# Optimization experiments

Measured on AMD Instinct MI355X. Metric: run time of the kernel, lower is better.

## Reference

```python
import jax, jax.numpy as jnp
import numpy as np

SPATIAL_SHAPES = np.array([[128, 128], [64, 64], [32, 32], [16, 16]], dtype=np.int32)  # (H, W) per level
D_MODEL = 256
D_FFN = 1024
N_LEVELS = 4
N_HEADS = 8
N_POINTS = 4
HEAD_DIM = D_MODEL // N_HEADS
B = 2
LEN = int((SPATIAL_SHAPES[:, 0] * SPATIAL_SHAPES[:, 1]).sum())  # 21760


def layer_norm(x, g, b, eps=1e-5):
    mu = x.mean(-1, keepdims=True)
    var = ((x - mu) ** 2).mean(-1, keepdims=True)
    return (x - mu) / jnp.sqrt(var + eps) * g + b


def ms_deform_attn_core(value, sampling_locations, attention_weights):
    # value: [B, Len, M, D]; locations: [B, Lq, M, L, P, 2] in [0,1]; weights: [B, Lq, M, L, P]
    B_, _, M, D = value.shape
    Lq = sampling_locations.shape[1]
    P = sampling_locations.shape[4]
    out = jnp.zeros((B_, M, Lq, D), value.dtype)
    start = 0
    for lvl, (H, W) in enumerate(SPATIAL_SHAPES.tolist()):
        v = value[:, start:start + H * W].transpose(0, 2, 1, 3)  # [B, M, H*W, D]
        start += H * W
        loc = sampling_locations[:, :, :, lvl].transpose(0, 2, 1, 3, 4)  # [B, M, Lq, P, 2]
        # grid_sample semantics: align_corners=False, padding_mode='zeros'
        x = loc[..., 0] * W - 0.5
        y = loc[..., 1] * H - 0.5
        x0 = jnp.floor(x)
        y0 = jnp.floor(y)
        wx = (x - x0)[..., None]
        wy = (y - y0)[..., None]

        def gather(xi, yi):
            valid = ((xi >= 0) & (xi < W) & (yi >= 0) & (yi < H)).astype(value.dtype)
            idx = (jnp.clip(yi, 0, H - 1) * W + jnp.clip(xi, 0, W - 1)).astype(jnp.int32)
            idx = idx.reshape(B_, M, Lq * P)
            g = jnp.take_along_axis(v, idx[..., None], axis=2).reshape(B_, M, Lq, P, D)
            return g * valid[..., None]

        v00 = gather(x0, y0)
        v01 = gather(x0 + 1, y0)
        v10 = gather(x0, y0 + 1)
        v11 = gather(x0 + 1, y0 + 1)
        samp = (v00 * (1 - wx) + v01 * wx) * (1 - wy) + (v10 * (1 - wx) + v11 * wx) * wy
        w_l = attention_weights[:, :, :, lvl].transpose(0, 2, 1, 3)  # [B, M, Lq, P]
        out = out + (samp * w_l[..., None]).sum(axis=3)
    return out.transpose(0, 2, 1, 3).reshape(B_, Lq, M * D)


def setup_inputs() -> dict:
    key = jax.random.key(0)
    ks = jax.random.split(key, 16)
    f32 = jnp.float32

    def lin(k, fan_in, fan_out, scale=None):
        s = scale if scale is not None else 1.0 / np.sqrt(fan_in)
        return jax.random.normal(k, (fan_in, fan_out), f32) * s

    starts = np.concatenate([[0], np.cumsum(SPATIAL_SHAPES[:, 0] * SPATIAL_SHAPES[:, 1])[:-1]]).astype(np.int32)
    inp = {
        "src": jax.random.normal(ks[0], (B, LEN, D_MODEL), f32),
        "pos": jax.random.normal(ks[1], (B, LEN, D_MODEL), f32),
        "reference_points": jax.random.uniform(ks[2], (B, LEN, N_LEVELS, 2), f32),
        "spatial_shapes": jnp.asarray(SPATIAL_SHAPES),
        "level_start_index": jnp.asarray(starts),
        "norm1_g": jnp.ones((D_MODEL,), f32), "norm1_b": jnp.zeros((D_MODEL,), f32),
        "norm2_g": jnp.ones((D_MODEL,), f32), "norm2_b": jnp.zeros((D_MODEL,), f32),
        "W_value": lin(ks[3], D_MODEL, D_MODEL), "b_value": jnp.zeros((D_MODEL,), f32),
        "W_off": lin(ks[4], D_MODEL, N_HEADS * N_LEVELS * N_POINTS * 2, scale=0.01),
        "b_off": jax.random.normal(ks[5], (N_HEADS * N_LEVELS * N_POINTS * 2,), f32) * 0.01,
        "W_attn": lin(ks[6], D_MODEL, N_HEADS * N_LEVELS * N_POINTS),
        "b_attn": jnp.zeros((N_HEADS * N_LEVELS * N_POINTS,), f32),
        "W_out": lin(ks[7], D_MODEL, D_MODEL), "b_out": jnp.zeros((D_MODEL,), f32),
        "W_ffn1": lin(ks[8], D_MODEL, D_FFN), "b_ffn1": jnp.zeros((D_FFN,), f32),
        "W_ffn2": lin(ks[9], D_FFN, D_MODEL), "b_ffn2": jnp.zeros((D_MODEL,), f32),
    }
    return inp


def reference(src, pos, reference_points, spatial_shapes, level_start_index,
              norm1_g, norm1_b, norm2_g, norm2_b,
              W_value, b_value, W_off, b_off, W_attn, b_attn, W_out, b_out,
              W_ffn1, b_ffn1, W_ffn2, b_ffn2):
    B_, Lq, C = src.shape
    # pre-norm deformable self-attention; NOTE: value path uses un-normed src (faithful to source)
    q = layer_norm(src, norm1_g, norm1_b) + pos
    value = (src @ W_value + b_value).reshape(B_, Lq, N_HEADS, HEAD_DIM)
    offsets = (q @ W_off + b_off).reshape(B_, Lq, N_HEADS, N_LEVELS, N_POINTS, 2)
    attn = jax.nn.softmax((q @ W_attn + b_attn).reshape(B_, Lq, N_HEADS, N_LEVELS * N_POINTS), axis=-1)
    attn = attn.reshape(B_, Lq, N_HEADS, N_LEVELS, N_POINTS)
    offset_normalizer = spatial_shapes[..., ::-1].astype(src.dtype)  # (W, H) per level
    loc = reference_points[:, :, None, :, None, :] + offsets / offset_normalizer[None, None, None, :, None, :]
    attn_out = ms_deform_attn_core(value, loc, attn) @ W_out + b_out
    src = src + attn_out
    h = layer_norm(src, norm2_g, norm2_b)
    h = jax.nn.gelu(h @ W_ffn1 + b_ffn1, approximate=False) @ W_ffn2 + b_ffn2
    return src + h
```

## Files before the change

### kernel.cpp

```cpp
#include <hip/hip_runtime.h>
#include <hip/hip_bf16.h>
#include <math.h>

#define LEN_TOT 21760
#define BATCH 2
#define MROWS (BATCH * LEN_TOT)
#define DMODEL 256
#define DFFN 1024

typedef unsigned short ushort_t;
typedef __attribute__((ext_vector_type(8))) short short8;
typedef __attribute__((ext_vector_type(4))) float floatx4;
typedef __attribute__((address_space(3))) ushort_t lds_us;
typedef __attribute__((address_space(1))) const ushort_t glb_us;

__device__ __forceinline__ ushort_t f2b(float f) {
    unsigned u = __float_as_uint(f);
    unsigned r = (u + 0x7FFFu + ((u >> 16) & 1u)) >> 16;
    return (ushort_t)r;
}

struct TP {
    const float* s[6];
    ushort_t*    d[6];
    int K[6];
    int N[6];
    int start[7];
};

__global__ __launch_bounds__(256) void transpose_convert(TP tp) {
    __shared__ float tile[32][33];
    int blk = blockIdx.x;
    int seg = 0;
    while (seg < 5 && blk >= tp.start[seg + 1]) seg++;
    int local = blk - tp.start[seg];
    int K = tp.K[seg], N = tp.N[seg];
    int tn = N >> 5;
    int k0 = (local / tn) << 5, n0 = (local % tn) << 5;
    int r = threadIdx.x >> 5, c = threadIdx.x & 31;
    const float* src = tp.s[seg];
    #pragma unroll
    for (int rr = r; rr < 32; rr += 8)
        tile[rr][c] = src[(size_t)(k0 + rr) * N + n0 + c];
    __syncthreads();
    ushort_t* dst = tp.d[seg];
    #pragma unroll
    for (int rr = r; rr < 32; rr += 8)
        dst[(size_t)(n0 + rr) * K + k0 + c] = f2b(tile[c][rr]);
}

__global__ __launch_bounds__(256) void ln_dual_kernel(
    const float* __restrict__ x, const float* __restrict__ g,
    const float* __restrict__ bb, const float* __restrict__ addv,
    ushort_t* __restrict__ y_bf, ushort_t* __restrict__ x_bf)
{
    int row  = blockIdx.x * 4 + (threadIdx.x >> 6);
    int lane = threadIdx.x & 63;
    size_t base = (size_t)row * DMODEL + lane * 4;
    float4 v = *(const float4*)(x + base);

    float s = v.x + v.y + v.z + v.w;
    #pragma unroll
    for (int o = 32; o; o >>= 1) s += __shfl_xor(s, o, 64);
    float mu = s * (1.0f / 256.0f);

    float d0 = v.x - mu, d1 = v.y - mu, d2 = v.z - mu, d3 = v.w - mu;
    float vs = d0*d0 + d1*d1 + d2*d2 + d3*d3;
    #pragma unroll
    for (int o = 32; o; o >>= 1) vs += __shfl_xor(vs, o, 64);
    float rstd = rsqrtf(vs * (1.0f / 256.0f) + 1e-5f);

    float4 gv = *(const float4*)(g  + lane * 4);
    float4 bv = *(const float4*)(bb + lane * 4);
    float o0 = d0 * rstd * gv.x + bv.x;
    float o1 = d1 * rstd * gv.y + bv.y;
    float o2 = d2 * rstd * gv.z + bv.z;
    float o3 = d3 * rstd * gv.w + bv.w;
    if (addv) {
        float4 av = *(const float4*)(addv + base);
        o0 += av.x; o1 += av.y; o2 += av.z; o3 += av.w;
    }
    ushort4 ob = {f2b(o0), f2b(o1), f2b(o2), f2b(o3)};
    *(ushort4*)(y_bf + base) = ob;
    if (x_bf) {
        ushort4 xb = {f2b(v.x), f2b(v.y), f2b(v.z), f2b(v.w)};
        *(ushort4*)(x_bf + base) = xb;
    }
}

template<int GELU_ACT, int HAS_RES, int OUT_BF16>
__global__ __launch_bounds__(256) void gemm_mfma(
    const ushort_t* __restrict__ A, const ushort_t* __restrict__ Bt,
    const float* __restrict__ bias, const float* __restrict__ res,
    float* __restrict__ C, ushort_t* __restrict__ Cbf,
    int M, int N, int K)
{
    constexpr int BM = 128, BK = 32;
    __shared__ __align__(16) ushort_t As[BM * BK];
    __shared__ __align__(16) ushort_t Bs[BM * BK];

    const int tid  = threadIdx.x;
    const int wave = tid >> 6;
    const int lane = tid & 63;
    const int wm = (wave & 1) * 64;
    const int wn = (wave >> 1) * 64;
    const int ml = lane & 15;
    const int quad = lane >> 4;
    const int m0 = blockIdx.y * BM, n0 = blockIdx.x * BM;

    const int r0 = tid >> 2, s0 = tid & 3;
    const int r1 = (tid + 256) >> 2;

    floatx4 acc[4][4] = {};

    for (int k0 = 0; k0 < K; k0 += BK) {
        const ushort_t* gA0 = A  + (size_t)(m0 + r0) * K + k0 + s0 * 8;
        const ushort_t* gA1 = A  + (size_t)(m0 + r1) * K + k0 + s0 * 8;
        const ushort_t* gB0 = Bt + (size_t)(n0 + r0) * K + k0 + s0 * 8;
        const ushort_t* gB1 = Bt + (size_t)(n0 + r1) * K + k0 + s0 * 8;
        __builtin_amdgcn_global_load_lds((glb_us*)gA0, (lds_us*)(As + tid * 8),        16, 0, 0);
        __builtin_amdgcn_global_load_lds((glb_us*)gA1, (lds_us*)(As + (tid + 256) * 8),16, 0, 0);
        __builtin_amdgcn_global_load_lds((glb_us*)gB0, (lds_us*)(Bs + tid * 8),        16, 0, 0);
        __builtin_amdgcn_global_load_lds((glb_us*)gB1, (lds_us*)(Bs + (tid + 256) * 8),16, 0, 0);
        __syncthreads();

        short8 af[4], bfr[4];
        #pragma unroll
        for (int i = 0; i < 4; i++)
            af[i] = *(const short8*)(As + (wm + i * 16 + ml) * BK + quad * 8);
        #pragma unroll
        for (int j = 0; j < 4; j++)
            bfr[j] = *(const short8*)(Bs + (wn + j * 16 + ml) * BK + quad * 8);
        #pragma unroll
        for (int i = 0; i < 4; i++)
            #pragma unroll
            for (int j = 0; j < 4; j++)
                acc[i][j] = __builtin_amdgcn_mfma_f32_16x16x32_bf16(
                    af[i], bfr[j], acc[i][j], 0, 0, 0);
        __syncthreads();
    }

    if (OUT_BF16) {
        ushort_t* pool  = (wave < 2) ? As : Bs;
        ushort_t* wbase = pool + (wave & 1) * 2048;
        const int lr  = lane >> 2;
        const int sg  = lane & 3;
        #pragma unroll
        for (int i = 0; i < 4; i++) {
            ushort_t* wbuf = wbase + (i & 1) * 1024;
            #pragma unroll
            for (int j = 0; j < 4; j++) {
                float bc = bias[n0 + wn + j * 16 + ml];
                #pragma unroll
                for (int r = 0; r < 4; r++) {
                    float v = acc[i][j][r] + bc;
                    if (GELU_ACT) v = 0.5f * v * (1.0f + erff(v * 0.7071067811865476f));
                    if (HAS_RES)
                        v += res[(size_t)(m0 + wm + i * 16 + quad * 4 + r) * N
                                 + n0 + wn + j * 16 + ml];
                    wbuf[(quad * 4 + r) * 64 + j * 16 + ml] = f2b(v);
                }
            }
            asm volatile("s_waitcnt lgkmcnt(0)" ::: "memory");
            #pragma unroll
            for (int h = 0; h < 2; h++) {
                short8 vv = *(const short8*)(wbuf + lr * 64 + (sg + 4 * h) * 8);
                *(short8*)(Cbf + (size_t)(m0 + wm + i * 16 + lr) * N
                                 + n0 + wn + (sg + 4 * h) * 8) = vv;
            }
        }
    } else {
        #pragma unroll
        for (int j = 0; j < 4; j++) {
            int col = n0 + wn + j * 16 + ml;
            float bc = bias[col];
            #pragma unroll
            for (int i = 0; i < 4; i++) {
                int row = m0 + wm + i * 16 + quad * 4;
                #pragma unroll
                for (int r = 0; r < 4; r++) {
                    float v = acc[i][j][r] + bc;
                    if (GELU_ACT) v = 0.5f * v * (1.0f + erff(v * 0.7071067811865476f));
                    if (HAS_RES) v += res[(size_t)(row + r) * N + col];
                    C[(size_t)(row + r) * N + col] = v;
                }
            }
        }
    }
}

__global__ __launch_bounds__(256) void msdeform_kernel(
    const float* __restrict__ value, const float* __restrict__ offs,
    const float* __restrict__ logits, const float* __restrict__ refp,
    ushort_t* __restrict__ out_bf)
{
    int gid = blockIdx.x * 8 + (threadIdx.x >> 5);
    int l   = threadIdx.x & 31;
    int bq  = gid >> 3;
    int m   = gid & 7;
    int b   = (bq >= LEN_TOT) ? 1 : 0;

    int i = l & 15;
    float logit = logits[(size_t)gid * 16 + i];
    float mx = logit;
    #pragma unroll
    for (int o = 8; o; o >>= 1) mx = fmaxf(mx, __shfl_xor(mx, o, 32));
    float e = __expf(logit - mx);
    float se = e;
    #pragma unroll
    for (int o = 8; o; o >>= 1) se += __shfl_xor(se, o, 32);
    float prob = e / se;

    int lvl = i >> 2;
    int Wl  = 128 >> lvl;
    float Wf = (float)Wl;
    const int ST_[4] = {0, 16384, 20480, 21504};

    float2 off2 = ((const float2*)offs)[(size_t)gid * 16 + i];
    float2 ref2 = ((const float2*)refp)[(size_t)bq * 4 + lvl];
    float xs = fmaf(ref2.x, Wf, off2.x) - 0.5f;
    float ys = fmaf(ref2.y, Wf, off2.y) - 0.5f;
    float xf = floorf(xs), yf = floorf(ys);
    int x0 = (int)xf, y0 = (int)yf;
    float wx = xs - xf, wy = ys - yf;
    float wx1 = 1.0f - wx, wy1 = 1.0f - wy;

    bool vx0 = (x0 >= 0) & (x0 < Wl);
    bool vx1 = (x0 + 1 >= 0) & (x0 + 1 < Wl);
    bool vy0 = (y0 >= 0) & (y0 < Wl);
    bool vy1 = (y0 + 1 >= 0) & (y0 + 1 < Wl);
    int cx0 = min(max(x0, 0), Wl - 1);
    int cx1 = min(max(x0 + 1, 0), Wl - 1);
    int cy0 = min(max(y0, 0), Wl - 1);
    int cy1 = min(max(y0 + 1, 0), Wl - 1);

    int vbase = b * LEN_TOT + ST_[lvl];
    int i00 = (vbase + cy0 * Wl + cx0) * 256 + m * 32;
    int i01 = (vbase + cy0 * Wl + cx1) * 256 + m * 32;
    int i10 = (vbase + cy1 * Wl + cx0) * 256 + m * 32;
    int i11 = (vbase + cy1 * Wl + cx1) * 256 + m * 32;
    float w00 = (vx0 && vy0) ? prob * wx1 * wy1 : 0.0f;
    float w01 = (vx1 && vy0) ? prob * wx  * wy1 : 0.0f;
    float w10 = (vx0 && vy1) ? prob * wx1 * wy  : 0.0f;
    float w11 = (vx1 && vy1) ? prob * wx  * wy  : 0.0f;

    int sA = l >> 2;
    int cA = l & 3;
    int t0 = __shfl(i00, sA, 32), t1 = __shfl(i01, sA, 32);
    int t2 = __shfl(i10, sA, 32), t3 = __shfl(i11, sA, 32);
    int addrA = (cA == 0) ? t0 : (cA == 1) ? t1 : (cA == 2) ? t2 : t3;
    float u0 = __shfl(w00, sA, 32), u1 = __shfl(w01, sA, 32);
    float u2 = __shfl(w10, sA, 32), u3 = __shfl(w11, sA, 32);
    float wA = (cA == 0) ? u0 : (cA == 1) ? u1 : (cA == 2) ? u2 : u3;
    t0 = __shfl(i00, sA + 8, 32); t1 = __shfl(i01, sA + 8, 32);
    t2 = __shfl(i10, sA + 8, 32); t3 = __shfl(i11, sA + 8, 32);
    int addrB = (cA == 0) ? t0 : (cA == 1) ? t1 : (cA == 2) ? t2 : t3;
    u0 = __shfl(w00, sA + 8, 32); u1 = __shfl(w01, sA + 8, 32);
    u2 = __shfl(w10, sA + 8, 32); u3 = __shfl(w11, sA + 8, 32);
    float wB = (cA == 0) ? u0 : (cA == 1) ? u1 : (cA == 2) ? u2 : u3;

    int cl = l >> 3;
    int d4 = l & 7;
    float ax = 0.0f, ay = 0.0f, az = 0.0f, aw = 0.0f;
    #pragma unroll
    for (int s = 0; s < 8; s++) {
        int   a = __shfl(addrA, s * 4 + cl, 32);
        float w = __shfl(wA,    s * 4 + cl, 32);
        float4 v = *(const float4*)(value + a + (d4 << 2));
        ax = fmaf(w, v.x, ax); ay = fmaf(w, v.y, ay);
        az = fmaf(w, v.z, az); aw = fmaf(w, v.w, aw);
    }
    #pragma unroll
    for (int s = 0; s < 8; s++) {
        int   a = __shfl(addrB, s * 4 + cl, 32);
        float w = __shfl(wB,    s * 4 + cl, 32);
        float4 v = *(const float4*)(value + a + (d4 << 2));
        ax = fmaf(w, v.x, ax); ay = fmaf(w, v.y, ay);
        az = fmaf(w, v.z, az); aw = fmaf(w, v.w, aw);
    }
    ax += __shfl_xor(ax, 8, 32);  ay += __shfl_xor(ay, 8, 32);
    az += __shfl_xor(az, 8, 32);  aw += __shfl_xor(aw, 8, 32);
    ax += __shfl_xor(ax, 16, 32); ay += __shfl_xor(ay, 16, 32);
    az += __shfl_xor(az, 16, 32); aw += __shfl_xor(aw, 16, 32);

    if (l < 8) {
        ushort4 o = {f2b(ax), f2b(ay), f2b(az), f2b(aw)};
        *(ushort4*)(out_bf + (size_t)gid * 32 + (d4 << 2)) = o;
    }
}

extern "C" void kernel_launch(void* const* d_in, const int* in_sizes, int n_in,
                              void* d_out, int out_size, void* d_ws, size_t ws_size,
                              hipStream_t stream)
{
    const float* src  = (const float*)d_in[0];
    const float* pos  = (const float*)d_in[1];
    const float* refp = (const float*)d_in[2];
    const float* n1g = (const float*)d_in[5];
    const float* n1b = (const float*)d_in[6];
    const float* n2g = (const float*)d_in[7];
    const float* n2b = (const float*)d_in[8];
    const float* Wv  = (const float*)d_in[9];
    const float* bv  = (const float*)d_in[10];
    const float* Wof = (const float*)d_in[11];
    const float* bof = (const float*)d_in[12];
    const float* Wat = (const float*)d_in[13];
    const float* bat = (const float*)d_in[14];
    const float* Wo  = (const float*)d_in[15];
    const float* bo  = (const float*)d_in[16];
    const float* Wf1 = (const float*)d_in[17];
    const float* bf1 = (const float*)d_in[18];
    const float* Wf2 = (const float*)d_in[19];
    const float* bf2 = (const float*)d_in[20];
    float* out = (float*)d_out;

    char* ws = (char*)d_ws;
    const int M = MROWS;
    const size_t SZ_BF = (size_t)M * 256 * 2;
    const size_t SZ_F  = (size_t)M * 256 * 4;

    ushort_t* q_bf    = (ushort_t*)(ws);
    float*    value   = (float*)   (ws + SZ_BF);
    ushort_t* src_bf  = (ushort_t*)(ws + SZ_BF + SZ_F);
    float*    offsb   = (float*)   (ws + 2 * SZ_BF + SZ_F);
    float*    logitsb = (float*)   (ws + 2 * SZ_BF + 2 * SZ_F);
    ushort_t* h0_bf   = q_bf;
    ushort_t* sampled = src_bf;
    float*    src2    = value;
    ushort_t* h1_bf   = src_bf;
    char* wtp = ws + 2 * SZ_BF + 2 * SZ_F + (size_t)M * 128 * 4;
    ushort_t* WvT  = (ushort_t*)(wtp);
    ushort_t* WofT = WvT  + 256 * 256;
    ushort_t* WatT = WofT + 256 * 256;
    ushort_t* WoT  = WatT + 256 * 128;
    ushort_t* Wf1T = WoT  + 256 * 256;
    ushort_t* Wf2T = Wf1T + 256 * 1024;

    TP tp;
    tp.s[0] = Wv;  tp.d[0] = WvT;  tp.K[0] = 256;  tp.N[0] = 256;
    tp.s[1] = Wof; tp.d[1] = WofT; tp.K[1] = 256;  tp.N[1] = 256;
    tp.s[2] = Wat; tp.d[2] = WatT; tp.K[2] = 256;  tp.N[2] = 128;
    tp.s[3] = Wo;  tp.d[3] = WoT;  tp.K[3] = 256;  tp.N[3] = 256;
    tp.s[4] = Wf1; tp.d[4] = Wf1T; tp.K[4] = 256;  tp.N[4] = 1024;
    tp.s[5] = Wf2; tp.d[5] = Wf2T; tp.K[5] = 1024; tp.N[5] = 256;
    tp.start[0] = 0;   tp.start[1] = 64;  tp.start[2] = 128;
    tp.start[3] = 160; tp.start[4] = 224; tp.start[5] = 480; tp.start[6] = 736;
    transpose_convert<<<736, 256, 0, stream>>>(tp);

    ln_dual_kernel<<<M / 4, 256, 0, stream>>>(src, n1g, n1b, pos, q_bf, src_bf);
    gemm_mfma<0, 0, 0><<<dim3(2, M / 128), 256, 0, stream>>>(
        src_bf, WvT, bv, nullptr, value, nullptr, M, 256, 256);
    gemm_mfma<0, 0, 0><<<dim3(2, M / 128), 256, 0, stream>>>(
        q_bf, WofT, bof, nullptr, offsb, nullptr, M, 256, 256);
    gemm_mfma<0, 0, 0><<<dim3(1, M / 128), 256, 0, stream>>>(
        q_bf, WatT, bat, nullptr, logitsb, nullptr, M, 128, 256);
    msdeform_kernel<<<M, 256, 0, stream>>>(value, offsb, logitsb, refp, sampled);
    gemm_mfma<0, 1, 0><<<dim3(2, M / 128), 256, 0, stream>>>(
        sampled, WoT, bo, src, src2, nullptr, M, 256, 256);
    ln_dual_kernel<<<M / 4, 256, 0, stream>>>(src2, n2g, n2b, nullptr, h0_bf, nullptr);
    gemm_mfma<1, 0, 1><<<dim3(8, M / 128), 256, 0, stream>>>(
        h0_bf, Wf1T, bf1, nullptr, nullptr, h1_bf, M, 1024, 256);
    gemm_mfma<0, 1, 0><<<dim3(2, M / 128), 256, 0, stream>>>(
        h1_bf, Wf2T, bf2, src2, out, nullptr, M, 256, 1024);
}
```

Measured before the change: 506.8 us.

## Fuse offset and attention-logit GEMMs and store value projection in bf16

The offset and attention-logit projections become one GEMM with N=384, which relies on WofT and WatT being contiguous and uses a split bias. Its output is a combined row-major buffer that the deformable-attention kernel indexes directly. The value projection now writes bf16 instead of fp32, which halves the gather traffic in msdeform_kernel, and loads are widened back to float in registers. The cost is lower precision in the sampled values and an extra branch on bias selection in every GEMM epilogue.

```diff
diff --git a/kernel.cpp b/kernel.cpp
--- a/kernel.cpp
+++ b/kernel.cpp
@@ -18,6 +18,9 @@
     unsigned u = __float_as_uint(f);
     unsigned r = (u + 0x7FFFu + ((u >> 16) & 1u)) >> 16;
     return (ushort_t)r;
+}
+__device__ __forceinline__ float b2f(ushort_t u) {
+    return __uint_as_float(((unsigned)u) << 16);
 }
 
 struct TP {
@@ -91,7 +94,8 @@
 template<int GELU_ACT, int HAS_RES, int OUT_BF16>
 __global__ __launch_bounds__(256) void gemm_mfma(
     const ushort_t* __restrict__ A, const ushort_t* __restrict__ Bt,
-    const float* __restrict__ bias, const float* __restrict__ res,
+    const float* __restrict__ bias, const float* __restrict__ bias2, int bsplit,
+    const float* __restrict__ res,
     float* __restrict__ C, ushort_t* __restrict__ Cbf,
     int M, int N, int K)
 {
@@ -150,7 +154,8 @@
             ushort_t* wbuf = wbase + (i & 1) * 1024;
             #pragma unroll
             for (int j = 0; j < 4; j++) {
-                float bc = bias[n0 + wn + j * 16 + ml];
+                int col = n0 + wn + j * 16 + ml;
+                float bc = (col < bsplit) ? bias[col] : bias2[col - bsplit];
                 #pragma unroll
                 for (int r = 0; r < 4; r++) {
                     float v = acc[i][j][r] + bc;
@@ -173,7 +178,7 @@
         #pragma unroll
         for (int j = 0; j < 4; j++) {
             int col = n0 + wn + j * 16 + ml;
-            float bc = bias[col];
+            float bc = (col < bsplit) ? bias[col] : bias2[col - bsplit];
             #pragma unroll
             for (int i = 0; i < 4; i++) {
                 int row = m0 + wm + i * 16 + quad * 4;
@@ -190,9 +195,8 @@
 }
 
 __global__ __launch_bounds__(256) void msdeform_kernel(
-    const float* __restrict__ value, const float* __restrict__ offs,
-    const float* __restrict__ logits, const float* __restrict__ refp,
-    ushort_t* __restrict__ out_bf)
+    const ushort_t* __restrict__ value, const float* __restrict__ comb,
+    const float* __restrict__ refp, ushort_t* __restrict__ out_bf)
 {
     int gid = blockIdx.x * 8 + (threadIdx.x >> 5);
     int l   = threadIdx.x & 31;
@@ -201,7 +205,7 @@
     int b   = (bq >= LEN_TOT) ? 1 : 0;
 
     int i = l & 15;
-    float logit = logits[(size_t)gid * 16 + i];
+    float logit = comb[(size_t)bq * 384 + 256 + m * 16 + i];
     float mx = logit;
     #pragma unroll
     for (int o = 8; o; o >>= 1) mx = fmaxf(mx, __shfl_xor(mx, o, 32));
@@ -216,7 +220,7 @@
     float Wf = (float)Wl;
     const int ST_[4] = {0, 16384, 20480, 21504};
 
-    float2 off2 = ((const float2*)offs)[(size_t)gid * 16 + i];
+    float2 off2 = ((const float2*)comb)[(size_t)bq * 192 + m * 16 + i];
     float2 ref2 = ((const float2*)refp)[(size_t)bq * 4 + lvl];
     float xs = fmaf(ref2.x, Wf, off2.x) - 0.5f;
     float ys = fmaf(ref2.y, Wf, off2.y) - 0.5f;
@@ -266,17 +270,17 @@
     for (int s = 0; s < 8; s++) {
         int   a = __shfl(addrA, s * 4 + cl, 32);
         float w = __shfl(wA,    s * 4 + cl, 32);
-        float4 v = *(const float4*)(value + a + (d4 << 2));
-        ax = fmaf(w, v.x, ax); ay = fmaf(w, v.y, ay);
-        az = fmaf(w, v.z, az); aw = fmaf(w, v.w, aw);
+        ushort4 v = *(const ushort4*)(value + a + (d4 << 2));
+        ax = fmaf(w, b2f(v.x), ax); ay = fmaf(w, b2f(v.y), ay);
+        az = fmaf(w, b2f(v.z), az); aw = fmaf(w, b2f(v.w), aw);
     }
     #pragma unroll
     for (int s = 0; s < 8; s++) {
         int   a = __shfl(addrB, s * 4 + cl, 32);
         float w = __shfl(wB,    s * 4 + cl, 32);
-        float4 v = *(const float4*)(value + a + (d4 << 2));
-        ax = fmaf(w, v.x, ax); ay = fmaf(w, v.y, ay);
-        az = fmaf(w, v.z, az); aw = fmaf(w, v.w, aw);
+        ushort4 v = *(const ushort4*)(value + a + (d4 << 2));
+        ax = fmaf(w, b2f(v.x), ax); ay = fmaf(w, b2f(v.y), ay);
+        az = fmaf(w, b2f(v.z), az); aw = fmaf(w, b2f(v.w), aw);
     }
     ax += __shfl_xor(ax, 8, 32);  ay += __shfl_xor(ay, 8, 32);
     az += __shfl_xor(az, 8, 32);  aw += __shfl_xor(aw, 8, 32);
@@ -318,15 +322,15 @@
     const int M = MROWS;
     const size_t SZ_BF = (size_t)M * 256 * 2;
     const size_t SZ_F  = (size_t)M * 256 * 4;
+    const int BIG = 1 << 30;
 
     ushort_t* q_bf    = (ushort_t*)(ws);
-    float*    value   = (float*)   (ws + SZ_BF);
+    ushort_t* value_b = (ushort_t*)(ws + SZ_BF);
     ushort_t* src_bf  = (ushort_t*)(ws + SZ_BF + SZ_F);
-    float*    offsb   = (float*)   (ws + 2 * SZ_BF + SZ_F);
-    float*    logitsb = (float*)   (ws + 2 * SZ_BF + 2 * SZ_F);
+    float*    comb    = (float*)   (ws + 2 * SZ_BF + SZ_F);
     ushort_t* h0_bf   = q_bf;
     ushort_t* sampled = src_bf;
-    float*    src2    = value;
+    float*    src2    = (float*)   (ws + SZ_BF);
     ushort_t* h1_bf   = src_bf;
     char* wtp = ws + 2 * SZ_BF + 2 * SZ_F + (size_t)M * 128 * 4;
     ushort_t* WvT  = (ushort_t*)(wtp);
@@ -348,18 +352,16 @@
     transpose_convert<<<736, 256, 0, stream>>>(tp);
 
     ln_dual_kernel<<<M / 4, 256, 0, stream>>>(src, n1g, n1b, pos, q_bf, src_bf);
-    gemm_mfma<0, 0, 0><<<dim3(2, M / 128), 256, 0, stream>>>(
-        src_bf, WvT, bv, nullptr, value, nullptr, M, 256, 256);
-    gemm_mfma<0, 0, 0><<<dim3(2, M / 128), 256, 0, stream>>>(
-        q_bf, WofT, bof, nullptr, offsb, nullptr, M, 256, 256);
-    gemm_mfma<0, 0, 0><<<dim3(1, M / 128), 256, 0, stream>>>(
-        q_bf, WatT, bat, nullptr, logitsb, nullptr, M, 128, 256);
-    msdeform_kernel<<<M, 256, 0, stream>>>(value, offsb, logitsb, refp, sampled);
+    gemm_mfma<0, 0, 1><<<dim3(2, M / 128), 256, 0, stream>>>(
+        src_bf, WvT, bv, bv, BIG, nullptr, nullptr, value_b, M, 256, 256);
+    gemm_mfma<0, 0, 0><<<dim3(3, M / 128), 256, 0, stream>>>(
+        q_bf, WofT, bof, bat, 256, nullptr, comb, nullptr, M, 384, 256);
+    msdeform_kernel<<<M, 256, 0, stream>>>(value_b, comb, refp, sampled);
     gemm_mfma<0, 1, 0><<<dim3(2, M / 128), 256, 0, stream>>>(
-        sampled, WoT, bo, src, src2, nullptr, M, 256, 256);
+        sampled, WoT, bo, bo, BIG, src, src2, nullptr, M, 256, 256);
     ln_dual_kernel<<<M / 4, 256, 0, stream>>>(src2, n2g, n2b, nullptr, h0_bf, nullptr);
     gemm_mfma<1, 0, 1><<<dim3(8, M / 128), 256, 0, stream>>>(
-        h0_bf, Wf1T, bf1, nullptr, nullptr, h1_bf, M, 1024, 256);
+        h0_bf, Wf1T, bf1, bf1, BIG, nullptr, nullptr, h1_bf, M, 1024, 256);
     gemm_mfma<0, 1, 0><<<dim3(2, M / 128), 256, 0, stream>>>(
-        h1_bf, Wf2T, bf2, src2, out, nullptr, M, 256, 1024);
-}
+        h1_bf, Wf2T, bf2, bf2, BIG, src2, out, nullptr, M, 256, 1024);
+}
```

New measurement: 500.3 us. About the same (-1.3%).
